# Kernel tuning notes

Hardware: AMD Instinct MI355X
Metric: run time of the kernel (lower is better)

Reference implementation:

```python
import jax, jax.numpy as jnp
import numpy as np

EPS = 1e-12

def _wn(v, g):
    # weight norm per output channel (axis 0): w[o] = g[o] * v[o] / ||v[o]||
    return g[:, None] * v / jnp.linalg.norm(v, axis=1, keepdims=True)

def _unit(x):
    # row-wise L2 normalize with clip, matching _normalize in source
    return x / jnp.clip(jnp.linalg.norm(x, axis=-1, keepdims=True), EPS)

def setup_inputs() -> dict:
    key = jax.random.key(0)
    ks = jax.random.split(key, 8)
    D, CD, K, T = 1024, 256, 8192, 16384
    return {
        "z": jax.random.normal(ks[0], (D, T), dtype=jnp.float32),
        "in_v": jax.random.normal(ks[1], (CD, D), dtype=jnp.float32) * 0.02,
        "in_g": jax.random.uniform(ks[2], (CD,), dtype=jnp.float32, minval=0.5, maxval=1.5),
        "in_b": jax.random.normal(ks[3], (CD,), dtype=jnp.float32) * 0.01,
        "out_v": jax.random.normal(ks[4], (D, CD), dtype=jnp.float32) * 0.02,
        "out_g": jax.random.uniform(ks[5], (D,), dtype=jnp.float32, minval=0.5, maxval=1.5),
        "out_b": jax.random.normal(ks[6], (D,), dtype=jnp.float32) * 0.01,
        "codebook": jax.random.normal(ks[7], (K, CD), dtype=jnp.float32),
    }

def reference(z, in_v, in_g, in_b, out_v, out_g, out_b, codebook):
    # in_proj: weight-normed 1x1 conv == matmul over channel dim
    z_e = _wn(in_v, in_g) @ z + in_b[:, None]            # (CD, T)
    # decode_latents
    enc = _unit(z_e.T)                                    # (T, CD)
    cb = _unit(codebook)                                  # (K, CD)
    # squared L2 distance via matmul-based cdist
    dist = (jnp.sum(enc * enc, axis=1, keepdims=True)
            - 2.0 * enc @ cb.T
            + jnp.sum(cb * cb, axis=1)[None, :])          # (T, K)
    indices = jnp.argmax(-dist, axis=1)                   # (T,)
    z_q = codebook[indices].T                             # (CD, T), raw codebook gather
    # straight-through estimator
    z_q = z_e + jax.lax.stop_gradient(z_q - z_e)
    # out_proj
    out = _wn(out_v, out_g) @ z_q + out_b[:, None]        # (D, T)
    return (out, indices)
```

## Files before the change

### kernel.cpp

```cpp
#include <hip/hip_runtime.h>
#include <hip/hip_bf16.h>
#include <math.h>

#define TDIM 16384
#define DDIM 1024
#define CDIM 256
#define KDIM 8192
#define KSPLIT 8

typedef unsigned short u16;
typedef __attribute__((ext_vector_type(8))) short bf16x8;
typedef __attribute__((ext_vector_type(8))) unsigned short us8;
typedef __attribute__((ext_vector_type(4))) float floatx4;

static const size_t OFF_WINH  = 0;
static const size_t OFF_WINL  = OFF_WINH  + (size_t)CDIM * DDIM / 2;
static const size_t OFF_WOUTH = OFF_WINL  + (size_t)CDIM * DDIM / 2;
static const size_t OFF_WOUTL = OFF_WOUTH + (size_t)DDIM * CDIM / 2;
static const size_t OFF_CBH   = OFF_WOUTL + (size_t)DDIM * CDIM / 2;
static const size_t OFF_CBL   = OFF_CBH   + (size_t)KDIM * CDIM / 2;
static const size_t OFF_C2    = OFF_CBL   + (size_t)KDIM * CDIM / 2;
static const size_t OFF_ZTH   = OFF_C2    + (size_t)KDIM;
static const size_t OFF_ZTL   = OFF_ZTH   + (size_t)TDIM * DDIM / 2;
static const size_t OFF_ZE    = OFF_ZTL   + (size_t)TDIM * DDIM / 2;
static const size_t OFF_PV    = OFF_ZE    + (size_t)CDIM * TDIM;
static const size_t OFF_PI    = OFF_PV    + (size_t)KSPLIT * TDIM;
static const size_t OFF_IDX   = OFF_PI    + (size_t)KSPLIT * TDIM;
static const size_t OFF_ETH   = OFF_ZTH;
static const size_t OFF_ETL   = OFF_ZTH + (size_t)TDIM * CDIM / 2;

static __device__ __forceinline__ u16 f2bf(float x) {
  __hip_bfloat16 h = __float2bfloat16(x);
  return *(u16*)&h;
}
static __device__ __forceinline__ float bf2f(u16 u) {
  __hip_bfloat16 h; *(u16*)&h = u;
  return __bfloat162float(h);
}

__global__ __launch_bounds__(256) void rownorm_split(
    const float* __restrict__ v, const float* __restrict__ g,
    u16* __restrict__ hi, u16* __restrict__ lo, float* __restrict__ c2,
    int ncols, int clip) {
  __shared__ float red[256];
  int row = blockIdx.x;
  const float* vr = v + (size_t)row * ncols;
  float s = 0.f;
  for (int j = threadIdx.x; j < ncols; j += 256) { float x = vr[j]; s += x * x; }
  red[threadIdx.x] = s;
  __syncthreads();
  for (int off = 128; off > 0; off >>= 1) {
    if (threadIdx.x < off) red[threadIdx.x] += red[threadIdx.x + off];
    __syncthreads();
  }
  float norm = sqrtf(red[0]);
  if (clip) norm = fmaxf(norm, 1e-12f);
  float scale = (g ? g[row] : 1.0f) / norm;
  float s2 = 0.f;
  for (int j = threadIdx.x; j < ncols; j += 256) {
    float y = vr[j] * scale;
    u16 hh = f2bf(y);
    u16 ll = f2bf(y - bf2f(hh));
    hi[(size_t)row * ncols + j] = hh;
    lo[(size_t)row * ncols + j] = ll;
    s2 += y * y;
  }
  if (c2) {
    __syncthreads();
    red[threadIdx.x] = s2;
    __syncthreads();
    for (int off = 128; off > 0; off >>= 1) {
      if (threadIdx.x < off) red[threadIdx.x] += red[threadIdx.x + off];
      __syncthreads();
    }
    if (threadIdx.x == 0) c2[row] = red[0];
  }
}

__global__ __launch_bounds__(256) void transpose_split_z(
    const float* __restrict__ z, u16* __restrict__ zth, u16* __restrict__ ztl) {
  __shared__ float tile[64][65];
  int t0 = blockIdx.x * 64, d0 = blockIdx.y * 64;
  int tl = threadIdx.x & 63, grp = threadIdx.x >> 6;
#pragma unroll
  for (int r = 0; r < 16; r++) {
    int d = grp * 16 + r;
    tile[d][tl] = z[(size_t)(d0 + d) * TDIM + t0 + tl];
  }
  __syncthreads();
#pragma unroll
  for (int r = 0; r < 16; r++) {
    int t = grp * 16 + r;
    float x = tile[tl][t];
    u16 h = f2bf(x);
    u16 l = f2bf(x - bf2f(h));
    zth[(size_t)(t0 + t) * DDIM + d0 + tl] = h;
    ztl[(size_t)(t0 + t) * DDIM + d0 + tl] = l;
  }
}

__global__ __launch_bounds__(256) void gemm_mfma_in(
    const u16* __restrict__ ah_g, const u16* __restrict__ al_g,
    const u16* __restrict__ bh_g, const u16* __restrict__ bl_g,
    const float* __restrict__ bias, float* __restrict__ C, int K) {
  __shared__ u16 Ah[128 * 32], Al[128 * 32];
  __shared__ u16 Bh[64 * 32],  Bl[64 * 32];
  int tid = threadIdx.x;
  int n0 = blockIdx.x * 64;
  int m0 = blockIdx.y * 128;
  int lane = tid & 63, wid = tid >> 6;
  int wr = wid >> 1, wc = wid & 1;
  int q = lane >> 4, mm = lane & 15;
  int h = tid & 1;
  int sr = ((tid >> 1) ^ (h << 2)) & 127;
  int ssw = (sr ^ (sr >> 2)) & 3;
  int o0 = sr * 32 + ((((h << 1))     ^ ssw) << 3);
  int o1 = sr * 32 + ((((h << 1) | 1) ^ ssw) << 3);
  int gcol = h * 16;
  int sb = ((tid >> 1) ^ (h << 2)) & 63;
  int ssb = (sb ^ (sb >> 2)) & 3;
  int p0 = sb * 32 + ((((h << 1))     ^ ssb) << 3);
  int p1 = sb * 32 + ((((h << 1) | 1) ^ ssb) << 3);
  int sm = (mm ^ (mm >> 2)) & 3;
  int cq = (q ^ sm) << 3;

  const floatx4 z4 = {0.f, 0.f, 0.f, 0.f};
  floatx4 acc[4][2];
#pragma unroll
  for (int i = 0; i < 4; i++)
#pragma unroll
    for (int j = 0; j < 2; j++) acc[i][j] = z4;

  for (int c0 = 0; c0 < K; c0 += 32) {
    const size_t ga = (size_t)(m0 + sr) * K + c0 + gcol;
    us8 a_h0 = *(const us8*)&ah_g[ga];
    us8 a_h1 = *(const us8*)&ah_g[ga + 8];
    us8 a_l0 = *(const us8*)&al_g[ga];
    us8 a_l1 = *(const us8*)&al_g[ga + 8];
    us8 b_h0, b_h1, b_l0, b_l1;
    if (tid < 128) {
      const size_t gb = (size_t)(n0 + sb) * K + c0 + gcol;
      b_h0 = *(const us8*)&bh_g[gb];
      b_h1 = *(const us8*)&bh_g[gb + 8];
      b_l0 = *(const us8*)&bl_g[gb];
      b_l1 = *(const us8*)&bl_g[gb + 8];
    }
    __syncthreads();
    *(us8*)&Ah[o0] = a_h0; *(us8*)&Ah[o1] = a_h1;
    *(us8*)&Al[o0] = a_l0; *(us8*)&Al[o1] = a_l1;
    if (tid < 128) {
      *(us8*)&Bh[p0] = b_h0; *(us8*)&Bh[p1] = b_h1;
      *(us8*)&Bl[p0] = b_l0; *(us8*)&Bl[p1] = b_l1;
    }
    __syncthreads();

    bf16x8 fa[4], fb[2];
#pragma unroll
    for (int i = 0; i < 4; i++)
      fa[i] = *(const bf16x8*)&Ah[(wr * 64 + i * 16 + mm) * 32 + cq];
#pragma unroll
    for (int j = 0; j < 2; j++)
      fb[j] = *(const bf16x8*)&Bh[(wc * 32 + j * 16 + mm) * 32 + cq];
#pragma unroll
    for (int i = 0; i < 4; i++)
#pragma unroll
      for (int j = 0; j < 2; j++)
        acc[i][j] = __builtin_amdgcn_mfma_f32_16x16x32_bf16(fa[i], fb[j], acc[i][j], 0, 0, 0);
#pragma unroll
    for (int i = 0; i < 4; i++) {
      bf16x8 fl = *(const bf16x8*)&Al[(wr * 64 + i * 16 + mm) * 32 + cq];
#pragma unroll
      for (int j = 0; j < 2; j++)
        acc[i][j] = __builtin_amdgcn_mfma_f32_16x16x32_bf16(fl, fb[j], acc[i][j], 0, 0, 0);
    }
#pragma unroll
    for (int j = 0; j < 2; j++) {
      bf16x8 fl = *(const bf16x8*)&Bl[(wc * 32 + j * 16 + mm) * 32 + cq];
#pragma unroll
      for (int i = 0; i < 4; i++)
        acc[i][j] = __builtin_amdgcn_mfma_f32_16x16x32_bf16(fa[i], fl, acc[i][j], 0, 0, 0);
    }
  }

#pragma unroll
  for (int i = 0; i < 4; i++) {
#pragma unroll
    for (int r = 0; r < 4; r++) {
      int m_loc = wr * 64 + i * 16 + q * 4 + r;
      float bb = bias[m0 + m_loc];
      float* crow = &C[(size_t)(m0 + m_loc) * TDIM + n0 + wc * 32 + mm];
#pragma unroll
      for (int j = 0; j < 2; j++) crow[j * 16] = acc[i][j][r] + bb;
    }
  }
}

__global__ __launch_bounds__(256) void gemm_mfma_bias(
    const u16* __restrict__ ah_g, const u16* __restrict__ al_g,
    const u16* __restrict__ bh_g, const u16* __restrict__ bl_g,
    const float* __restrict__ bias, float* __restrict__ C, int K) {
  __shared__ u16 Ah[128 * 32], Al[128 * 32];
  __shared__ u16 Bh[128 * 32], Bl[128 * 32];
  int tid = threadIdx.x;
  int n0 = blockIdx.x * 128;
  int m0 = blockIdx.y * 128;
  int lane = tid & 63, wid = tid >> 6;
  int wr = wid >> 1, wc = wid & 1;
  int q = lane >> 4, mm = lane & 15;
  int h = tid & 1;
  int sr = ((tid >> 1) ^ (h << 2)) & 127;
  int ssw = (sr ^ (sr >> 2)) & 3;
  int o0 = sr * 32 + ((((h << 1))     ^ ssw) << 3);
  int o1 = sr * 32 + ((((h << 1) | 1) ^ ssw) << 3);
  int gcol = h * 16;
  int sm = (mm ^ (mm >> 2)) & 3;
  int cq = (q ^ sm) << 3;

  const floatx4 z4 = {0.f, 0.f, 0.f, 0.f};
  floatx4 acc[4][4];
#pragma unroll
  for (int i = 0; i < 4; i++)
#pragma unroll
    for (int j = 0; j < 4; j++) acc[i][j] = z4;

  for (int c0 = 0; c0 < K; c0 += 32) {
    const size_t ga = (size_t)(m0 + sr) * K + c0 + gcol;
    const size_t gb = (size_t)(n0 + sr) * K + c0 + gcol;
    us8 a_h0 = *(const us8*)&ah_g[ga];
    us8 a_h1 = *(const us8*)&ah_g[ga + 8];
    us8 a_l0 = *(const us8*)&al_g[ga];
    us8 a_l1 = *(const us8*)&al_g[ga + 8];
    us8 b_h0 = *(const us8*)&bh_g[gb];
    us8 b_h1 = *(const us8*)&bh_g[gb + 8];
    us8 b_l0 = *(const us8*)&bl_g[gb];
    us8 b_l1 = *(const us8*)&bl_g[gb + 8];
    __syncthreads();
    *(us8*)&Ah[o0] = a_h0; *(us8*)&Ah[o1] = a_h1;
    *(us8*)&Al[o0] = a_l0; *(us8*)&Al[o1] = a_l1;
    *(us8*)&Bh[o0] = b_h0; *(us8*)&Bh[o1] = b_h1;
    *(us8*)&Bl[o0] = b_l0; *(us8*)&Bl[o1] = b_l1;
    __syncthreads();

    bf16x8 fa[4], fb[4];
#pragma unroll
    for (int i = 0; i < 4; i++)
      fa[i] = *(const bf16x8*)&Ah[(wr * 64 + i * 16 + mm) * 32 + cq];
#pragma unroll
    for (int j = 0; j < 4; j++)
      fb[j] = *(const bf16x8*)&Bh[(wc * 64 + j * 16 + mm) * 32 + cq];
#pragma unroll
    for (int i = 0; i < 4; i++)
#pragma unroll
      for (int j = 0; j < 4; j++)
        acc[i][j] = __builtin_amdgcn_mfma_f32_16x16x32_bf16(fa[i], fb[j], acc[i][j], 0, 0, 0);
#pragma unroll
    for (int i = 0; i < 4; i++) {
      bf16x8 fl = *(const bf16x8*)&Al[(wr * 64 + i * 16 + mm) * 32 + cq];
#pragma unroll
      for (int j = 0; j < 4; j++)
        acc[i][j] = __builtin_amdgcn_mfma_f32_16x16x32_bf16(fl, fb[j], acc[i][j], 0, 0, 0);
    }
#pragma unroll
    for (int j = 0; j < 4; j++) {
      bf16x8 fl = *(const bf16x8*)&Bl[(wc * 64 + j * 16 + mm) * 32 + cq];
#pragma unroll
      for (int i = 0; i < 4; i++)
        acc[i][j] = __builtin_amdgcn_mfma_f32_16x16x32_bf16(fa[i], fl, acc[i][j], 0, 0, 0);
    }
  }

#pragma unroll
  for (int i = 0; i < 4; i++) {
#pragma unroll
    for (int r = 0; r < 4; r++) {
      int m_loc = wr * 64 + i * 16 + q * 4 + r;
      float bb = bias[m0 + m_loc];
      float* crow = &C[(size_t)(m0 + m_loc) * TDIM + n0 + wc * 64 + mm];
#pragma unroll
      for (int j = 0; j < 4; j++) crow[j * 16] = acc[i][j][r] + bb;
    }
  }
}

__global__ __launch_bounds__(256) void finish_ze(
    const float* __restrict__ ze, u16* __restrict__ eth, u16* __restrict__ etl) {
  __shared__ float tile[256][33];
  __shared__ float red[8][32];
  __shared__ float invs[32];
  int t0 = blockIdx.x * 32;
  int tl = threadIdx.x & 31, grp = threadIdx.x >> 5;
  float s = 0.f;
  for (int c = grp * 32; c < grp * 32 + 32; c++) {
    float v = ze[(size_t)c * TDIM + t0 + tl];
    tile[c][tl] = v;
    s += v * v;
  }
  red[grp][tl] = s;
  __syncthreads();
  if (grp == 0) {
    float tot = 0.f;
#pragma unroll
    for (int gg = 0; gg < 8; gg++) tot += red[gg][tl];
    invs[tl] = 1.0f / fmaxf(sqrtf(tot), 1e-12f);
  }
  __syncthreads();
#pragma unroll
  for (int r = 0; r < 4; r++) {
    int t = grp * 4 + r;
    float iv = invs[t];
#pragma unroll
    for (int cc = 0; cc < 8; cc++) {
      int cd = cc * 32 + tl;
      float x = tile[cd][t] * iv;
      u16 hh = f2bf(x);
      u16 ll = f2bf(x - bf2f(hh));
      eth[(size_t)(t0 + t) * CDIM + cd] = hh;
      etl[(size_t)(t0 + t) * CDIM + cd] = ll;
    }
  }
}

__global__ __launch_bounds__(512, 2) void dist_mfma(
    const u16* __restrict__ eth, const u16* __restrict__ etl,
    const u16* __restrict__ cbh, const u16* __restrict__ cbl,
    const float* __restrict__ c2, float* __restrict__ pv, int* __restrict__ pi) {
  __shared__ u16 Bh[128 * 256];
  __shared__ u16 Ah[2][256 * 32];
  __shared__ u16 Al[2][256 * 32];
  __shared__ u16 Bls[2][128 * 32];
  __shared__ float mv[4][128];
  __shared__ int   mi[4][128];

  int tid = threadIdx.x;
  int t0 = blockIdx.x * 128;
  int kbeg = blockIdx.y * (KDIM / KSPLIT);
  int lane = tid & 63, wid = tid >> 6;
  int wk = wid >> 1, wt = wid & 1;
  int q = lane >> 4, mm = lane & 15;
  int sm2 = (mm ^ (mm >> 2)) & 3;
  int cq2 = (q ^ sm2) << 3;
  int sm5 = sm2 | (((mm >> 1) & 1) << 2);

  int rA = tid >> 2;
  int gA = tid & 3;
  int sswA = (rA ^ (rA >> 2)) & 3;
  int colA = (gA ^ sswA) << 3;
  int ldsA = rA * 32 + (gA << 3);

  for (int it = 0; it < 8; ++it) {
    int gi = it * 512 + tid;
    int r = gi >> 5, p5 = gi & 31;
    int f5 = ((r ^ (r >> 2)) & 3) | (((r >> 1) & 1) << 2);
    us8 v = *(const us8*)&eth[(size_t)(t0 + r) * CDIM + ((p5 ^ f5) << 3)];
    *(us8*)&Bh[r * 256 + (p5 << 3)] = v;
  }

  {
    const size_t ga = (size_t)(kbeg + rA) * CDIM + colA;
    us8 ah0 = *(const us8*)&cbh[ga];
    us8 ah1 = *(const us8*)&cbh[ga + (size_t)128 * CDIM];
    us8 al0 = *(const us8*)&cbl[ga];
    us8 al1 = *(const us8*)&cbl[ga + (size_t)128 * CDIM];
    us8 bl0 = *(const us8*)&etl[(size_t)(t0 + rA) * CDIM + colA];
    *(us8*)&Ah[0][ldsA] = ah0; *(us8*)&Ah[0][ldsA + 4096] = ah1;
    *(us8*)&Al[0][ldsA] = al0; *(us8*)&Al[0][ldsA + 4096] = al1;
    *(us8*)&Bls[0][ldsA] = bl0;
  }
  __syncthreads();

  float rbv[4]; int rbi[4];
#pragma unroll
  for (int j = 0; j < 4; j++) { rbv[j] = INFINITY; rbi[j] = 0x7fffffff; }

  const floatx4 z4 = {0.f, 0.f, 0.f, 0.f};
  floatx4 acc[4][4];
#pragma unroll
  for (int i = 0; i < 4; i++)
#pragma unroll
    for (int j = 0; j < 4; j++) acc[i][j] = z4;

  int cur = 0;
  for (int n = 0; n < 32; ++n) {
    int cc = n & 7;

    us8 ah0, ah1, al0, al1, bl0;
    if (n < 31) {
      int n1 = n + 1;
      int k0n = kbeg + (n1 >> 3) * 256;
      int c0n = (n1 & 7) * 32;
      const size_t ga = (size_t)(k0n + rA) * CDIM + c0n + colA;
      ah0 = *(const us8*)&cbh[ga];
      ah1 = *(const us8*)&cbh[ga + (size_t)128 * CDIM];
      al0 = *(const us8*)&cbl[ga];
      al1 = *(const us8*)&cbl[ga + (size_t)128 * CDIM];
      bl0 = *(const us8*)&etl[(size_t)(t0 + rA) * CDIM + c0n + colA];
    }

    bf16x8 fah[4], fbh[4];
#pragma unroll
    for (int i = 0; i < 4; i++)
      fah[i] = *(const bf16x8*)&Ah[cur][(wk * 64 + i * 16 + mm) * 32 + cq2];
#pragma unroll
    for (int j = 0; j < 4; j++)
      fbh[j] = *(const bf16x8*)&Bh[(wt * 64 + j * 16 + mm) * 256 +
                                   ((((cc << 2) | q) ^ sm5) << 3)];
#pragma unroll
    for (int i = 0; i < 4; i++)
#pragma unroll
      for (int j = 0; j < 4; j++)
        acc[i][j] = __builtin_amdgcn_mfma_f32_16x16x32_bf16(fah[i], fbh[j], acc[i][j], 0, 0, 0);
#pragma unroll
    for (int i = 0; i < 4; i++) {
      bf16x8 fl = *(const bf16x8*)&Al[cur][(wk * 64 + i * 16 + mm) * 32 + cq2];
#pragma unroll
      for (int j = 0; j < 4; j++)
        acc[i][j] = __builtin_amdgcn_mfma_f32_16x16x32_bf16(fl, fbh[j], acc[i][j], 0, 0, 0);
    }
#pragma unroll
    for (int j = 0; j < 4; j++) {
      bf16x8 fl = *(const bf16x8*)&Bls[cur][(wt * 64 + j * 16 + mm) * 32 + cq2];
#pragma unroll
      for (int i = 0; i < 4; i++)
        acc[i][j] = __builtin_amdgcn_mfma_f32_16x16x32_bf16(fah[i], fl, acc[i][j], 0, 0, 0);
    }

    if (n < 31) {
      int nb = cur ^ 1;
      *(us8*)&Ah[nb][ldsA] = ah0; *(us8*)&Ah[nb][ldsA + 4096] = ah1;
      *(us8*)&Al[nb][ldsA] = al0; *(us8*)&Al[nb][ldsA + 4096] = al1;
      *(us8*)&Bls[nb][ldsA] = bl0;
    }
    __syncthreads();
    cur ^= 1;

    if (cc == 7) {
      int k0 = kbeg + (n >> 3) * 256;
#pragma unroll
      for (int i = 0; i < 4; i++) {
#pragma unroll
        for (int r4 = 0; r4 < 4; r4++) {
          int kg = k0 + wk * 64 + i * 16 + q * 4 + r4;
          float c2v = c2[kg];
#pragma unroll
          for (int j = 0; j < 4; j++) {
            float s = c2v - 2.0f * acc[i][j][r4];
            if (s < rbv[j]) { rbv[j] = s; rbi[j] = kg; }
          }
        }
      }
#pragma unroll
      for (int i = 0; i < 4; i++)
#pragma unroll
        for (int j = 0; j < 4; j++) acc[i][j] = z4;
    }
  }

#pragma unroll
  for (int j = 0; j < 4; j++) {
    float v = rbv[j]; int ii = rbi[j];
    float ov = __shfl_xor(v, 16, 64); int oi = __shfl_xor(ii, 16, 64);
    if (ov < v || (ov == v && oi < ii)) { v = ov; ii = oi; }
    ov = __shfl_xor(v, 32, 64); oi = __shfl_xor(ii, 32, 64);
    if (ov < v || (ov == v && oi < ii)) { v = ov; ii = oi; }
    rbv[j] = v; rbi[j] = ii;
  }
  if (q == 0) {
#pragma unroll
    for (int j = 0; j < 4; j++) {
      mv[wk][wt * 64 + j * 16 + mm] = rbv[j];
      mi[wk][wt * 64 + j * 16 + mm] = rbi[j];
    }
  }
  __syncthreads();
  if (tid < 128) {
    float v0 = mv[0][tid]; int i0 = mi[0][tid];
#pragma unroll
    for (int w = 1; w < 4; w++) {
      float v1 = mv[w][tid]; int i1 = mi[w][tid];
      if (v1 < v0 || (v1 == v0 && i1 < i0)) { v0 = v1; i0 = i1; }
    }
    pv[(size_t)blockIdx.y * TDIM + t0 + tid] = v0;
    pi[(size_t)blockIdx.y * TDIM + t0 + tid] = i0;
  }
}

__global__ __launch_bounds__(256) void merge_argmin(
    const float* __restrict__ pv, const int* __restrict__ pi,
    int* __restrict__ idx, float* __restrict__ idxf) {
  int t = blockIdx.x * 256 + threadIdx.x;
  float bv = INFINITY; int bi = 0x7fffffff;
  for (int s = 0; s < KSPLIT; s++) {
    float v = pv[(size_t)s * TDIM + t];
    int ii = pi[(size_t)s * TDIM + t];
    if (v < bv || (v == bv && ii < bi)) { bv = v; bi = ii; }
  }
  idx[t] = bi;
  idxf[t] = (float)bi;
}

__global__ __launch_bounds__(256) void gather_split(
    const int* __restrict__ idx, const float* __restrict__ cb,
    u16* __restrict__ zqh, u16* __restrict__ zql) {
  int t = blockIdx.x * 4 + (threadIdx.x >> 6);
  int c4 = (threadIdx.x & 63) * 4;
  int k = idx[t];
  float4 x = *(const float4*)&cb[(size_t)k * CDIM + c4];
  u16 h0 = f2bf(x.x), h1 = f2bf(x.y), h2 = f2bf(x.z), h3 = f2bf(x.w);
  u16 l0 = f2bf(x.x - bf2f(h0)), l1 = f2bf(x.y - bf2f(h1));
  u16 l2 = f2bf(x.z - bf2f(h2)), l3 = f2bf(x.w - bf2f(h3));
  ushort4 hv = {h0, h1, h2, h3}, lv = {l0, l1, l2, l3};
  *(ushort4*)&zqh[(size_t)t * CDIM + c4] = hv;
  *(ushort4*)&zql[(size_t)t * CDIM + c4] = lv;
}

extern "C" void kernel_launch(void* const* d_in, const int* in_sizes, int n_in,
                              void* d_out, int out_size, void* d_ws, size_t ws_size,
                              hipStream_t stream) {
  const float* z     = (const float*)d_in[0];
  const float* in_v  = (const float*)d_in[1];
  const float* in_g  = (const float*)d_in[2];
  const float* in_b  = (const float*)d_in[3];
  const float* out_v = (const float*)d_in[4];
  const float* out_g = (const float*)d_in[5];
  const float* out_b = (const float*)d_in[6];
  const float* cb    = (const float*)d_in[7];

  float* ws    = (float*)d_ws;
  u16*   winh  = (u16*)(ws + OFF_WINH);
  u16*   winl  = (u16*)(ws + OFF_WINL);
  u16*   wouth = (u16*)(ws + OFF_WOUTH);
  u16*   woutl = (u16*)(ws + OFF_WOUTL);
  u16*   cbh   = (u16*)(ws + OFF_CBH);
  u16*   cbl   = (u16*)(ws + OFF_CBL);
  float* c2    = ws + OFF_C2;
  u16*   zth   = (u16*)(ws + OFF_ZTH);
  u16*   ztl   = (u16*)(ws + OFF_ZTL);
  float* z_e   = ws + OFF_ZE;
  float* pv    = ws + OFF_PV;
  int*   pi    = (int*)(ws + OFF_PI);
  int*   idxw  = (int*)(ws + OFF_IDX);
  u16*   eth   = (u16*)(ws + OFF_ETH);
  u16*   etl   = (u16*)(ws + OFF_ETL);
  u16*   zqh   = eth;
  u16*   zql   = etl;

  float* outp = (float*)d_out;
  float* idxf = outp + (size_t)DDIM * TDIM;

  rownorm_split<<<CDIM, 256, 0, stream>>>(in_v, in_g, winh, winl, nullptr, DDIM, 0);
  rownorm_split<<<DDIM, 256, 0, stream>>>(out_v, out_g, wouth, woutl, nullptr, CDIM, 0);
  rownorm_split<<<KDIM, 256, 0, stream>>>(cb, nullptr, cbh, cbl, c2, CDIM, 1);

  transpose_split_z<<<dim3(TDIM / 64, DDIM / 64), 256, 0, stream>>>(z, zth, ztl);

  gemm_mfma_in<<<dim3(TDIM / 64, CDIM / 128), 256, 0, stream>>>(
      winh, winl, zth, ztl, in_b, z_e, DDIM);

  finish_ze<<<TDIM / 32, 256, 0, stream>>>(z_e, eth, etl);

  dist_mfma<<<dim3(TDIM / 128, KSPLIT), 512, 0, stream>>>(eth, etl, cbh, cbl, c2, pv, pi);
  merge_argmin<<<TDIM / 256, 256, 0, stream>>>(pv, pi, idxw, idxf);

  gather_split<<<TDIM / 4, 256, 0, stream>>>(idxw, cb, zqh, zql);

  gemm_mfma_bias<<<dim3(TDIM / 128, DDIM / 128), 256, 0, stream>>>(
      wouth, woutl, zqh, zql, out_b, outp, CDIM);
}
```

Baseline: 435.1 us.

## Stream codebook tiles via direct global-to-LDS loads and read enc fragments from global

Restructures the distance kernel's memory plan. Codebook hi/lo tiles are now copied with global_load_lds (direct to shared memory) in 64-wide K chunks, double buffered, with an XOR swizzle. The encoding hi/lo fragments are loaded straight from global memory into registers each iteration instead of being staged in LDS. This drops the register round-trip for codebook staging and halves the number of barriers. The cost is repeated global (L2-cached) reads of the encoding data, more registers for the fragment arrays, and a per-iteration barrier that now comes after the argmin update.

```diff
diff --git a/kernel.cpp b/kernel.cpp
--- a/kernel.cpp
+++ b/kernel.cpp
@@ -36,6 +36,12 @@
 static __device__ __forceinline__ float bf2f(u16 u) {
   __hip_bfloat16 h; *(u16*)&h = u;
   return __bfloat162float(h);
+}
+
+static __device__ __forceinline__ void gload16(const u16* g, u16* l) {
+  __builtin_amdgcn_global_load_lds(
+      (__attribute__((address_space(1))) void*)g,
+      (__attribute__((address_space(3))) void*)l, 16, 0, 0);
 }
 
 __global__ __launch_bounds__(256) void rownorm_split(
@@ -324,10 +330,8 @@
     const u16* __restrict__ eth, const u16* __restrict__ etl,
     const u16* __restrict__ cbh, const u16* __restrict__ cbl,
     const float* __restrict__ c2, float* __restrict__ pv, int* __restrict__ pi) {
-  __shared__ u16 Bh[128 * 256];
-  __shared__ u16 Ah[2][256 * 32];
-  __shared__ u16 Al[2][256 * 32];
-  __shared__ u16 Bls[2][128 * 32];
+  __shared__ u16 AhL[2][256 * 64];
+  __shared__ u16 AlL[2][256 * 64];
   __shared__ float mv[4][128];
   __shared__ int   mi[4][128];
 
@@ -337,36 +341,21 @@
   int lane = tid & 63, wid = tid >> 6;
   int wk = wid >> 1, wt = wid & 1;
   int q = lane >> 4, mm = lane & 15;
-  int sm2 = (mm ^ (mm >> 2)) & 3;
-  int cq2 = (q ^ sm2) << 3;
-  int sm5 = sm2 | (((mm >> 1) & 1) << 2);
-
-  int rA = tid >> 2;
-  int gA = tid & 3;
-  int sswA = (rA ^ (rA >> 2)) & 3;
-  int colA = (gA ^ sswA) << 3;
-  int ldsA = rA * 32 + (gA << 3);
-
-  for (int it = 0; it < 8; ++it) {
+
+  int stR[4], stC[4], stL[4];
+#pragma unroll
+  for (int it = 0; it < 4; it++) {
     int gi = it * 512 + tid;
-    int r = gi >> 5, p5 = gi & 31;
-    int f5 = ((r ^ (r >> 2)) & 3) | (((r >> 1) & 1) << 2);
-    us8 v = *(const us8*)&eth[(size_t)(t0 + r) * CDIM + ((p5 ^ f5) << 3)];
-    *(us8*)&Bh[r * 256 + (p5 << 3)] = v;
-  }
-
-  {
-    const size_t ga = (size_t)(kbeg + rA) * CDIM + colA;
-    us8 ah0 = *(const us8*)&cbh[ga];
-    us8 ah1 = *(const us8*)&cbh[ga + (size_t)128 * CDIM];
-    us8 al0 = *(const us8*)&cbl[ga];
-    us8 al1 = *(const us8*)&cbl[ga + (size_t)128 * CDIM];
-    us8 bl0 = *(const us8*)&etl[(size_t)(t0 + rA) * CDIM + colA];
-    *(us8*)&Ah[0][ldsA] = ah0; *(us8*)&Ah[0][ldsA + 4096] = ah1;
-    *(us8*)&Al[0][ldsA] = al0; *(us8*)&Al[0][ldsA + 4096] = al1;
-    *(us8*)&Bls[0][ldsA] = bl0;
-  }
-  __syncthreads();
+    int r = gi >> 3, g = gi & 7;
+    stR[it] = r;
+    stC[it] = (g ^ (r & 7)) << 3;
+    stL[it] = gi << 3;
+  }
+
+  int foff[2];
+#pragma unroll
+  for (int kk = 0; kk < 2; kk++)
+    foff[kk] = ((((kk << 2) | q) ^ (mm & 7)) << 3);
 
   float rbv[4]; int rbi[4];
 #pragma unroll
@@ -379,62 +368,69 @@
 #pragma unroll
     for (int j = 0; j < 4; j++) acc[i][j] = z4;
 
-  int cur = 0;
-  for (int n = 0; n < 32; ++n) {
-    int cc = n & 7;
-
-    us8 ah0, ah1, al0, al1, bl0;
-    if (n < 31) {
+#pragma unroll
+  for (int it = 0; it < 4; it++) {
+    const size_t ga = (size_t)(kbeg + stR[it]) * CDIM + stC[it];
+    gload16(&cbh[ga], &AhL[0][stL[it]]);
+    gload16(&cbl[ga], &AlL[0][stL[it]]);
+  }
+  __syncthreads();
+
+  for (int n = 0; n < 16; ++n) {
+    int b = n & 1;
+    int c0 = (n & 3) * 64;
+
+    bf16x8 fbh[4][2], fbl[4][2];
+#pragma unroll
+    for (int j = 0; j < 4; j++) {
+      const size_t gb = (size_t)(t0 + wt * 64 + j * 16 + mm) * CDIM + c0 + q * 8;
+#pragma unroll
+      for (int kk = 0; kk < 2; kk++) {
+        fbh[j][kk] = *(const bf16x8*)&eth[gb + kk * 32];
+        fbl[j][kk] = *(const bf16x8*)&etl[gb + kk * 32];
+      }
+    }
+
+    if (n < 15) {
       int n1 = n + 1;
-      int k0n = kbeg + (n1 >> 3) * 256;
-      int c0n = (n1 & 7) * 32;
-      const size_t ga = (size_t)(k0n + rA) * CDIM + c0n + colA;
-      ah0 = *(const us8*)&cbh[ga];
-      ah1 = *(const us8*)&cbh[ga + (size_t)128 * CDIM];
-      al0 = *(const us8*)&cbl[ga];
-      al1 = *(const us8*)&cbl[ga + (size_t)128 * CDIM];
-      bl0 = *(const us8*)&etl[(size_t)(t0 + rA) * CDIM + c0n + colA];
-    }
-
-    bf16x8 fah[4], fbh[4];
-#pragma unroll
-    for (int i = 0; i < 4; i++)
-      fah[i] = *(const bf16x8*)&Ah[cur][(wk * 64 + i * 16 + mm) * 32 + cq2];
-#pragma unroll
-    for (int j = 0; j < 4; j++)
-      fbh[j] = *(const bf16x8*)&Bh[(wt * 64 + j * 16 + mm) * 256 +
-                                   ((((cc << 2) | q) ^ sm5) << 3)];
-#pragma unroll
-    for (int i = 0; i < 4; i++)
-#pragma unroll
-      for (int j = 0; j < 4; j++)
-        acc[i][j] = __builtin_amdgcn_mfma_f32_16x16x32_bf16(fah[i], fbh[j], acc[i][j], 0, 0, 0);
-#pragma unroll
-    for (int i = 0; i < 4; i++) {
-      bf16x8 fl = *(const bf16x8*)&Al[cur][(wk * 64 + i * 16 + mm) * 32 + cq2];
-#pragma unroll
-      for (int j = 0; j < 4; j++)
-        acc[i][j] = __builtin_amdgcn_mfma_f32_16x16x32_bf16(fl, fbh[j], acc[i][j], 0, 0, 0);
-    }
-#pragma unroll
-    for (int j = 0; j < 4; j++) {
-      bf16x8 fl = *(const bf16x8*)&Bls[cur][(wt * 64 + j * 16 + mm) * 32 + cq2];
+      int k0n = kbeg + (n1 >> 2) * 256;
+      int c0n = (n1 & 3) * 64;
+#pragma unroll
+      for (int it = 0; it < 4; it++) {
+        const size_t ga = (size_t)(k0n + stR[it]) * CDIM + c0n + stC[it];
+        gload16(&cbh[ga], &AhL[b ^ 1][stL[it]]);
+        gload16(&cbl[ga], &AlL[b ^ 1][stL[it]]);
+      }
+    }
+
+#pragma unroll
+    for (int kk = 0; kk < 2; kk++) {
+      bf16x8 fah[4];
 #pragma unroll
       for (int i = 0; i < 4; i++)
-        acc[i][j] = __builtin_amdgcn_mfma_f32_16x16x32_bf16(fah[i], fl, acc[i][j], 0, 0, 0);
-    }
-
-    if (n < 31) {
-      int nb = cur ^ 1;
-      *(us8*)&Ah[nb][ldsA] = ah0; *(us8*)&Ah[nb][ldsA + 4096] = ah1;
-      *(us8*)&Al[nb][ldsA] = al0; *(us8*)&Al[nb][ldsA + 4096] = al1;
-      *(us8*)&Bls[nb][ldsA] = bl0;
-    }
-    __syncthreads();
-    cur ^= 1;
-
-    if (cc == 7) {
-      int k0 = kbeg + (n >> 3) * 256;
+        fah[i] = *(const bf16x8*)&AhL[b][(wk * 64 + i * 16 + mm) * 64 + foff[kk]];
+#pragma unroll
+      for (int i = 0; i < 4; i++)
+#pragma unroll
+        for (int j = 0; j < 4; j++)
+          acc[i][j] = __builtin_amdgcn_mfma_f32_16x16x32_bf16(fah[i], fbh[j][kk], acc[i][j], 0, 0, 0);
+#pragma unroll
+      for (int i = 0; i < 4; i++) {
+        bf16x8 fl = *(const bf16x8*)&AlL[b][(wk * 64 + i * 16 + mm) * 64 + foff[kk]];
+#pragma unroll
+        for (int j = 0; j < 4; j++)
+          acc[i][j] = __builtin_amdgcn_mfma_f32_16x16x32_bf16(fl, fbh[j][kk], acc[i][j], 0, 0, 0);
+      }
+#pragma unroll
+      for (int j = 0; j < 4; j++) {
+#pragma unroll
+        for (int i = 0; i < 4; i++)
+          acc[i][j] = __builtin_amdgcn_mfma_f32_16x16x32_bf16(fah[i], fbl[j][kk], acc[i][j], 0, 0, 0);
+      }
+    }
+
+    if ((n & 3) == 3) {
+      int k0 = kbeg + (n >> 2) * 256;
 #pragma unroll
       for (int i = 0; i < 4; i++) {
 #pragma unroll
@@ -453,6 +449,8 @@
 #pragma unroll
         for (int j = 0; j < 4; j++) acc[i][j] = z4;
     }
+
+    __syncthreads();
   }
 
 #pragma unroll
```

Measured after the change: 573.4 us. 1.32x slower.
